# Optimization experiments

Measured on AMD Instinct MI355X. Metric: run time of the kernel, lower is better.

Reference implementation:

```python
import jax, jax.numpy as jnp
import numpy as np

B, S, D, T = 64, 128, 512, 64  # batch, encoder len, dim_model, longest_coor

def setup_inputs() -> dict:
    key = jax.random.key(0)
    ks = jax.random.split(key, 10)
    def rn(k, shape, s=0.02):
        return jax.random.normal(k, shape, dtype=jnp.float32) * s
    return dict(
        e_all=jax.random.normal(ks[0], (B, S, D), dtype=jnp.float32),
        e_last=jax.random.normal(ks[1], (1, B, D), dtype=jnp.float32),
        Wa_w=rn(ks[2], (D, D)), Wa_b=jnp.zeros((D,), jnp.float32),
        Ua_w=rn(ks[3], (D, D)), Ua_b=jnp.zeros((D,), jnp.float32),
        Va_w=rn(ks[4], (D, 1)), Va_b=jnp.zeros((1,), jnp.float32),
        W_ih=rn(ks[5], (3 * D, D + 3)),  # GRU input weights, input = cat(attn[D], coord[3])
        W_hh=rn(ks[6], (3 * D, D)),
        b_ih=jnp.zeros((3 * D,), jnp.float32),
        b_hh=jnp.zeros((3 * D,), jnp.float32),
        Wo_w=rn(ks[7], (D, 3)), Wo_b=jnp.zeros((3,), jnp.float32),
    )

def reference(e_all, e_last, Wa_w, Wa_b, Ua_w, Ua_b, Va_w, Va_b,
              W_ih, W_hh, b_ih, b_hh, Wo_w, Wo_b):
    # Ua(keys) is step-invariant: hoist out of the decode loop (same math).
    Uk = e_all @ Ua_w + Ua_b                      # [B,S,D]
    h0 = e_last[0]                                # [B,D]
    x0 = jnp.zeros((e_all.shape[0], 3), e_all.dtype)

    def step(carry, _):
        h, x = carry
        # Bahdanau attention: query = current hidden state
        q = h @ Wa_w + Wa_b                       # [B,D]
        scores = jnp.squeeze(jnp.tanh(q[:, None, :] + Uk) @ Va_w, -1) + Va_b  # [B,S]
        w = jax.nn.softmax(scores, axis=-1)       # [B,S]
        ctx = jnp.einsum('bs,bsd->bd', w, e_all)  # [B,D]
        # single-step GRU, input = cat(context, prev coord)
        gin = jnp.concatenate([ctx, x], axis=-1)  # [B,D+3]
        gi = gin @ W_ih.T + b_ih                  # [B,3D]
        gh = h @ W_hh.T + b_hh                    # [B,3D]
        gir, giz, gin_n = jnp.split(gi, 3, axis=-1)
        ghr, ghz, ghn = jnp.split(gh, 3, axis=-1)
        r = jax.nn.sigmoid(gir + ghr)
        z = jax.nn.sigmoid(giz + ghz)
        n = jnp.tanh(gin_n + r * ghn)
        h_new = (1.0 - z) * n + z * h             # [B,D]
        out = h_new @ Wo_w + Wo_b                 # [B,3]
        return (h_new, out), (out, w)

    (hT, _), (outs, attns) = jax.lax.scan(step, (h0, x0), None, length=T)
    d_outputs = jnp.transpose(outs, (1, 0, 2))    # [B,T,3]
    cross_attn = jnp.transpose(attns, (1, 0, 2))  # [B,T,S]
    return d_outputs, hT[None], cross_attn
```

## Files before the change

kernel.cpp:

```cpp
#include <hip/hip_runtime.h>

typedef unsigned int u32;
typedef unsigned long long u64;
typedef float f32x4 __attribute__((ext_vector_type(4)));
typedef short short8 __attribute__((ext_vector_type(8)));

#define OFF_UKB 0u
#define OFF_QX  16777216u
#define OFF_EX  17563648u
#define G_BYTES 102400u

#define OFF_OUT_HT  12288u
#define OFF_OUT_ATT 45056u

#define NBLK 192
#define NTHR 512
#define DYN_LDS 145408
#define PREP_LDS 36864

__device__ __forceinline__ float fast_rcp(float x) { return __builtin_amdgcn_rcpf(x); }
__device__ __forceinline__ float tanh5(float x) {
    float e = __expf(2.f * x);
    return 1.f - 2.f * fast_rcp(e + 1.f);
}
__device__ __forceinline__ float sigm_f(float x) { return fast_rcp(1.f + __expf(-x)); }

__device__ __forceinline__ u32 packbf2(float a, float b) {
    u32 ua = __float_as_uint(a); ua += 0x7FFFu + ((ua >> 16) & 1u);
    u32 ub = __float_as_uint(b); ub += 0x7FFFu + ((ub >> 16) & 1u);
    return (ua >> 16) | (ub & 0xFFFF0000u);
}
__device__ __forceinline__ float2 unpackbf2(u32 u) {
    return make_float2(__uint_as_float(u << 16), __uint_as_float(u & 0xFFFF0000u));
}
__device__ __forceinline__ float bf16hi(float x, float& lo) {
    u32 u = __float_as_uint(x); u += 0x7FFFu + ((u >> 16) & 1u); u &= 0xFFFF0000u;
    const float h = __uint_as_float(u); lo = x - h; return h;
}

__device__ __forceinline__ u64 cload64(const u64* p) {
    return __hip_atomic_load(p, __ATOMIC_RELAXED, __HIP_MEMORY_SCOPE_AGENT);
}
__device__ __forceinline__ void cstore64(u64* p, u64 v) {
    __hip_atomic_store(p, v, __ATOMIC_RELAXED, __HIP_MEMORY_SCOPE_AGENT);
}
__device__ __forceinline__ u32 cload32(const u32* p) {
    return __hip_atomic_load(p, __ATOMIC_RELAXED, __HIP_MEMORY_SCOPE_AGENT);
}
__device__ __forceinline__ void cstore32(u32* p, u32 v) {
    __hip_atomic_store(p, v, __ATOMIC_RELAXED, __HIP_MEMORY_SCOPE_AGENT);
}

union U8 { u32 u[4]; uint4 q; short8 s; };

__global__ __launch_bounds__(256) void prep_kernel(
    const float* __restrict__ e_all, const float* __restrict__ e_last,
    const float* __restrict__ Ua_w,  const float* __restrict__ Ua_b,
    float* __restrict__ ws)
{
    extern __shared__ char pls[];
    u32* Ahi = (u32*)pls;
    u32* Alo = Ahi + 64 * 36;
    u32* Bhi = Alo + 64 * 36;
    u32* Blo = Bhi + 64 * 36;

    u32* UKB = (u32*)((char*)ws + OFF_UKB);

    const int blk = blockIdx.x, tid = threadIdx.x;
    const int gtid = blk * 256 + tid, gstride = 1024 * 256;

    for (int i = gtid; i < 2048; i += gstride) {
        const int g = i >> 9, j = i & 511;
        ((u32*)((char*)ws + OFF_EX + (size_t)g * G_BYTES + 98304))[j] = 0u;
    }
    for (int i = gtid; i < 32768; i += gstride) {
        const int g = i >> 13, j = i & 8191;
        ((u64*)((char*)ws + OFF_EX + (size_t)g * G_BYTES + 32768))[j] = 0ull;
    }
    for (int i = gtid; i < 65536; i += gstride)
        ((u64*)((char*)ws + OFF_QX))[i] = 0ull;
    for (int i = gtid; i < 8192; i += gstride) {
        const int g = i >> 11, i2 = i & 2047;
        const float* ep = e_last + ((size_t)(g * 16 + (i2 >> 7)) * 512) + 4 * (i2 & 127);
        u64* HX = (u64*)((char*)ws + OFF_EX + (size_t)g * G_BYTES);
        HX[i2] = (u64)packbf2(ep[0], ep[1]) | ((u64)packbf2(ep[2], ep[3]) << 32);
    }

    const int r0 = (blk >> 3) * 64, c0 = (blk & 7) * 64;
    const int lane = tid & 63, wv = tid >> 6;
    const int mn = lane & 15, quad = lane >> 4;

    f32x4 acc[4];
    #pragma unroll
    for (int rg = 0; rg < 4; ++rg) acc[rg] = (f32x4){0.f, 0.f, 0.f, 0.f};

    for (int ks = 0; ks < 8; ++ks) {
        if (ks) __syncthreads();
        for (int i = tid; i < 1024; i += 256) {
            const int row = i >> 4, q4i = i & 15;
            const float4 e = *(const float4*)(e_all + (size_t)(r0 + row) * 512 + ks * 64 + 4 * q4i);
            float l0, l1, l2, l3;
            const float h0 = bf16hi(e.x, l0), h1 = bf16hi(e.y, l1);
            const float h2 = bf16hi(e.z, l2), h3 = bf16hi(e.w, l3);
            Ahi[row * 36 + 2 * q4i]     = packbf2(h0, h1);
            Ahi[row * 36 + 2 * q4i + 1] = packbf2(h2, h3);
            Alo[row * 36 + 2 * q4i]     = packbf2(l0, l1);
            Alo[row * 36 + 2 * q4i + 1] = packbf2(l2, l3);
        }
        for (int i = tid; i < 2048; i += 256) {
            const int col = i & 63, kp = i >> 6;
            const float b0 = Ua_w[(size_t)(ks * 64 + 2 * kp) * 512 + c0 + col];
            const float b1 = Ua_w[(size_t)(ks * 64 + 2 * kp + 1) * 512 + c0 + col];
            float l0, l1;
            const float h0 = bf16hi(b0, l0), h1 = bf16hi(b1, l1);
            Bhi[col * 36 + kp] = packbf2(h0, h1);
            Blo[col * 36 + kp] = packbf2(l0, l1);
        }
        __syncthreads();
        #pragma unroll
        for (int kb = 0; kb < 2; ++kb) {
            const int fo = kb * 16 + quad * 4;
            U8 bh, bl;
            bh.q = *(const uint4*)(Bhi + (wv * 16 + mn) * 36 + fo);
            bl.q = *(const uint4*)(Blo + (wv * 16 + mn) * 36 + fo);
            #pragma unroll
            for (int rg = 0; rg < 4; ++rg) {
                U8 ah, al;
                ah.q = *(const uint4*)(Ahi + (rg * 16 + mn) * 36 + fo);
                al.q = *(const uint4*)(Alo + (rg * 16 + mn) * 36 + fo);
                acc[rg] = __builtin_amdgcn_mfma_f32_16x16x32_bf16(al.s, bh.s, acc[rg], 0, 0, 0);
                acc[rg] = __builtin_amdgcn_mfma_f32_16x16x32_bf16(ah.s, bl.s, acc[rg], 0, 0, 0);
                acc[rg] = __builtin_amdgcn_mfma_f32_16x16x32_bf16(ah.s, bh.s, acc[rg], 0, 0, 0);
            }
        }
    }
    const int col = c0 + wv * 16 + mn;
    const float bias = Ua_b[col];
    #pragma unroll
    for (int rg = 0; rg < 4; ++rg) {
        #pragma unroll
        for (int reg = 0; reg < 4; ++reg) {
            const float v = acc[rg][reg] + bias;
            const float v1 = __shfl_down(v, 1);
            if (!(mn & 1))
                UKB[(size_t)(r0 + rg * 16 + quad * 4 + reg) * 256 + (col >> 1)] = packbf2(v, v1);
        }
    }
}

__global__ __launch_bounds__(512, 1) void decode_kernel(
    const float* __restrict__ e_all,
    const float* __restrict__ e_last,
    const float* __restrict__ Wa_w,  const float* __restrict__ Wa_b,
    const float* __restrict__ Va_w,
    const float* __restrict__ W_ih,  const float* __restrict__ W_hh,
    const float* __restrict__ b_ih,  const float* __restrict__ b_hh,
    const float* __restrict__ Wo_w,  const float* __restrict__ Wo_b,
    float* __restrict__ out, float* __restrict__ ws)
{
    extern __shared__ char smraw[];

    const u32* UKB = (const u32*)((char*)ws + OFF_UKB);

    const int tid = threadIdx.x;
    const int bi  = blockIdx.x;
    const int g   = bi / 48, r = bi % 48;
    const int lane = tid & 63, wv = tid >> 6;

    char* gbase = (char*)ws + OFF_EX + (size_t)g * G_BYTES;
    u64* HX = (u64*)gbase;
    u64* CX = (u64*)(gbase + 32768);
    u32* FH = (u32*)(gbase + 98304);

    if (r < 16) {
        const int bl = r, b = g * 16 + bl;
        u32*   EuL  = (u32*)smraw;
        float* eq_s = (float*)(smraw + 131072);
        float* w_s  = (float*)(smraw + 133120);
        float* red  = (float*)(smraw + 133632);
        float* psq  = (float*)(smraw + 133696);

        const u64* QXR = (const u64*)((char*)ws + OFF_QX + (size_t)g * 131072u);

        {
            const uint4* src = (const uint4*)(UKB + (size_t)b * 32768);
            uint4* dst = (uint4*)EuL;
            #pragma unroll
            for (int i = 0; i < 16; ++i) {
                uint4 u = src[tid + 512 * i];
                float2 p;
                p = unpackbf2(u.x); u.x = packbf2(__expf(2.f * p.x), __expf(2.f * p.y));
                p = unpackbf2(u.y); u.y = packbf2(__expf(2.f * p.x), __expf(2.f * p.y));
                p = unpackbf2(u.z); u.z = packbf2(__expf(2.f * p.x), __expf(2.f * p.y));
                p = unpackbf2(u.w); u.w = packbf2(__expf(2.f * p.x), __expf(2.f * p.y));
                dst[tid + 512 * i] = u;
            }
        }
        uint2 ereg[32];
        {
            const int dq = tid & 127, sg = tid >> 7;
            const float* ep = e_all + (size_t)b * 65536;
            #pragma unroll
            for (int si = 0; si < 32; ++si) {
                const float4 e = *(const float4*)(ep + (size_t)(sg * 32 + si) * 512 + 4 * dq);
                ereg[si] = make_uint2(packbf2(e.x, e.y), packbf2(e.z, e.w));
            }
        }
        const int kl = lane & 15;
        float4 va2a[4], va2b[4];
        float vaSum = 0.f;
        #pragma unroll
        for (int it = 0; it < 4; ++it) {
            const float4 a  = *(const float4*)(Va_w + (it * 16 + kl) * 8);
            const float4 b2 = *(const float4*)(Va_w + (it * 16 + kl) * 8 + 4);
            vaSum += a.x + a.y + a.z + a.w + b2.x + b2.y + b2.z + b2.w;
            va2a[it] = make_float4(-2.f * a.x,  -2.f * a.y,  -2.f * a.z,  -2.f * a.w);
            va2b[it] = make_float4(-2.f * b2.x, -2.f * b2.y, -2.f * b2.z, -2.f * b2.w);
        }
        __syncthreads();

        for (int t = 0; t < 64; ++t) {
            const int slot = t & 1;
            const u32 tg = (u32)(t + 1);
            u64* CxS = CX + slot * 4096;
            const u64* QxS = QXR + slot * 8192 + (size_t)bl * 512;

            if (tid < 256) {
                u64 v0 = cload64(QxS + 2 * tid), v1 = cload64(QxS + 2 * tid + 1);
                while ((u32)(v0 >> 32) != tg) v0 = cload64(QxS + 2 * tid);
                while ((u32)(v1 >> 32) != tg) v1 = cload64(QxS + 2 * tid + 1);
                ((float2*)eq_s)[tid] = make_float2(__uint_as_float((u32)v0),
                                                   __uint_as_float((u32)v1));
            }
            __syncthreads();

            {
                float4 eqa[4], eqb[4];
                const float4* q4 = (const float4*)eq_s;
                #pragma unroll
                for (int it = 0; it < 4; ++it) {
                    eqa[it] = q4[(it * 16 + kl) * 2];  eqb[it] = q4[(it * 16 + kl) * 2 + 1];
                }
                const int sbase = wv * 16 + (lane >> 4);
                #pragma unroll
                for (int sg = 0; sg < 4; ++sg) {
                    const int s = sbase + sg * 4;
                    const uint4* uk4 = (const uint4*)EuL + (size_t)s * 64;
                    float acc = vaSum;
                    #pragma unroll
                    for (int it = 0; it < 4; ++it) {
                        const uint4 u = uk4[it * 16 + kl];
                        const float2 u0 = unpackbf2(u.x), u1 = unpackbf2(u.y);
                        const float2 u2 = unpackbf2(u.z), u3 = unpackbf2(u.w);
                        acc = fmaf(va2a[it].x, fast_rcp(fmaf(eqa[it].x, u0.x, 1.f)), acc);
                        acc = fmaf(va2a[it].y, fast_rcp(fmaf(eqa[it].y, u0.y, 1.f)), acc);
                        acc = fmaf(va2a[it].z, fast_rcp(fmaf(eqa[it].z, u1.x, 1.f)), acc);
                        acc = fmaf(va2a[it].w, fast_rcp(fmaf(eqa[it].w, u1.y, 1.f)), acc);
                        acc = fmaf(va2b[it].x, fast_rcp(fmaf(eqb[it].x, u2.x, 1.f)), acc);
                        acc = fmaf(va2b[it].y, fast_rcp(fmaf(eqb[it].y, u2.y, 1.f)), acc);
                        acc = fmaf(va2b[it].z, fast_rcp(fmaf(eqb[it].z, u3.x, 1.f)), acc);
                        acc = fmaf(va2b[it].w, fast_rcp(fmaf(eqb[it].w, u3.y, 1.f)), acc);
                    }
                    acc += __shfl_xor(acc, 1); acc += __shfl_xor(acc, 2);
                    acc += __shfl_xor(acc, 4); acc += __shfl_xor(acc, 8);
                    if (kl == 0) w_s[s] = __expf(acc);
                }
            }
            __syncthreads();

            if (tid < 64) {
                float sm = w_s[tid] + w_s[tid + 64];
                #pragma unroll
                for (int off = 32; off > 0; off >>= 1) sm += __shfl_down(sm, off);
                if (tid == 0) red[1] = fast_rcp(sm);
            }
            {
                const int dq = tid & 127, sg = tid >> 7;
                float4 a = {0.f, 0.f, 0.f, 0.f};
                #pragma unroll
                for (int si = 0; si < 32; ++si) {
                    const float wgt = w_s[sg * 32 + si];
                    const float2 e0 = unpackbf2(ereg[si].x), e1 = unpackbf2(ereg[si].y);
                    a.x = fmaf(wgt, e0.x, a.x);
                    a.y = fmaf(wgt, e0.y, a.y);
                    a.z = fmaf(wgt, e1.x, a.z);
                    a.w = fmaf(wgt, e1.y, a.w);
                }
                ((float4*)psq)[sg * 128 + dq] = a;
            }
            __syncthreads();
            if (tid < 128) {
                const float rn = red[1];
                const float4* p4 = (const float4*)psq;
                float4 a = p4[tid], b2 = p4[128 + tid], c2 = p4[256 + tid], d2 = p4[384 + tid];
                const float rx = (a.x + b2.x + c2.x + d2.x) * rn;
                const float ry = (a.y + b2.y + c2.y + d2.y) * rn;
                const float rz = (a.z + b2.z + c2.z + d2.z) * rn;
                const float rw = (a.w + b2.w + c2.w + d2.w) * rn;
                const u64 tg64 = (u64)tg << 32;
                cstore64(CxS + (size_t)bl * 256 + 2 * tid,     tg64 | (u64)packbf2(rx, ry));
                cstore64(CxS + (size_t)bl * 256 + 2 * tid + 1, tg64 | (u64)packbf2(rz, rw));
            } else if (tid < 256) {
                out[OFF_OUT_ATT + ((size_t)b * 64 + t) * 128 + (tid - 128)] = w_s[tid - 128] * red[1];
            }
        }
    } else {
        const int idx = r - 16, d0 = idx * 16;
        u32*   hbu  = (u32*)smraw;
        u32*   cbu  = (u32*)(smraw + 16640);
        float* gh_s = (float*)(smraw + 33280);
        float* gi_s = (float*)(smraw + 36352);
        float* x_s  = (float*)(smraw + 39424);
        float* wx_s = (float*)(smraw + 39616);
        float* wo_s = (float*)(smraw + 40192);

        u64* QXW = (u64*)((char*)ws + OFF_QX + (size_t)g * 131072u);

        const int mn = lane & 15, quad = lane >> 4;

        short8 bfrag[16];
        float qbias = 0.f;
        if (wv < 3) {
            const float* wrow = W_hh + (size_t)(wv * 512 + d0 + mn) * 512;
            #pragma unroll
            for (int kb = 0; kb < 16; ++kb) {
                const int k0 = kb * 32 + quad * 8;
                U8 tpk;
                #pragma unroll
                for (int c = 0; c < 4; ++c)
                    tpk.u[c] = packbf2(wrow[k0 + 2 * c], wrow[k0 + 2 * c + 1]);
                bfrag[kb] = tpk.s;
            }
        } else if (wv < 6) {
            const float* wrow = W_ih + (size_t)((wv - 3) * 512 + d0 + mn) * 515;
            #pragma unroll
            for (int kb = 0; kb < 16; ++kb) {
                const int k0 = kb * 32 + quad * 8;
                U8 tpk;
                #pragma unroll
                for (int c = 0; c < 4; ++c)
                    tpk.u[c] = packbf2(wrow[k0 + 2 * c], wrow[k0 + 2 * c + 1]);
                bfrag[kb] = tpk.s;
            }
        } else if (wv == 6) {
            #pragma unroll
            for (int kb = 0; kb < 16; ++kb) {
                const int k0 = kb * 32 + quad * 8;
                U8 tpk;
                #pragma unroll
                for (int c = 0; c < 4; ++c)
                    tpk.u[c] = packbf2(Wa_w[(size_t)(k0 + 2 * c) * 512 + d0 + mn],
                                       Wa_w[(size_t)(k0 + 2 * c + 1) * 512 + d0 + mn]);
                bfrag[kb] = tpk.s;
            }
            qbias = Wa_b[d0 + mn];
        }
        if (tid < 144) {
            const int dd = tid / 9, rem = tid - dd * 9, g3 = rem / 3, c = rem - g3 * 3;
            wx_s[tid] = W_ih[(size_t)(g3 * 512 + d0 + dd) * 515 + 512 + c];
        }
        for (int i = tid; i < 1536; i += 512) wo_s[i] = Wo_w[i];
        if (tid < 3) wo_s[1536 + tid] = Wo_b[tid];

        const int gb = tid >> 4, gd = tid & 15;
        float hold = 0.f, bih[3], bhh[3];
        if (tid < 256) {
            hold = e_last[(size_t)(g * 16 + gb) * 512 + d0 + gd];
            #pragma unroll
            for (int g3 = 0; g3 < 3; ++g3) {
                bih[g3] = b_ih[g3 * 512 + d0 + gd];
                bhh[g3] = b_hh[g3 * 512 + d0 + gd];
            }
        }

        for (int t = 0; t < 64; ++t) {
            const int slot = t & 1;
            const u32 tg = (u32)(t + 1);
            const u64* HxS = HX + slot * 2048;
            const u64* CxS = CX + slot * 4096;
            u64* HxW = HX + ((t + 1) & 1) * 2048;

            if (lane < 16) {
                const u32* f = FH + ((wv & 1) * 16 + lane) * 16;
                while (cload32(f) < (u32)t) {}
            }
            #pragma unroll
            for (int u = 0; u < 4; ++u) {
                const int i = tid + 512 * u;
                const u64 v = cload64(HxS + i);
                *(u64*)(hbu + (i >> 7) * 260 + (i & 127) * 2) = v;
            }
            __syncthreads();

            if (wv < 3) {
                f32x4 c = {0.f, 0.f, 0.f, 0.f};
                #pragma unroll
                for (int kb = 0; kb < 16; ++kb) {
                    U8 a; a.q = *(const uint4*)(hbu + mn * 260 + kb * 16 + quad * 4);
                    c = __builtin_amdgcn_mfma_f32_16x16x32_bf16(a.s, bfrag[kb], c, 0, 0, 0);
                }
                #pragma unroll
                for (int reg = 0; reg < 4; ++reg)
                    gh_s[((quad * 4 + reg) * 16 + mn) * 3 + wv] = c[reg];
            } else if (wv == 7) {
                const int tt = tid - 448, cb = tt >> 2, kl = tt & 3;
                if (t > 0) {
                    float a0 = 0.f, a1 = 0.f, a2 = 0.f;
                    #pragma unroll 4
                    for (int c = 0; c < 64; ++c) {
                        const int p = kl * 64 + c;
                        const float2 hv = unpackbf2(hbu[cb * 260 + p]);
                        const float* w0 = wo_s + 2 * p * 3;
                        a0 = fmaf(hv.x, w0[0], fmaf(hv.y, w0[3], a0));
                        a1 = fmaf(hv.x, w0[1], fmaf(hv.y, w0[4], a1));
                        a2 = fmaf(hv.x, w0[2], fmaf(hv.y, w0[5], a2));
                    }
                    a0 += __shfl_xor(a0, 1); a1 += __shfl_xor(a1, 1); a2 += __shfl_xor(a2, 1);
                    a0 += __shfl_xor(a0, 2); a1 += __shfl_xor(a1, 2); a2 += __shfl_xor(a2, 2);
                    if (kl == 0) {
                        x_s[cb * 3 + 0] = a0 + wo_s[1536];
                        x_s[cb * 3 + 1] = a1 + wo_s[1537];
                        x_s[cb * 3 + 2] = a2 + wo_s[1538];
                    }
                } else if (tt < 48) x_s[tt] = 0.f;
            } else {
                if (wv == 6) {
                    f32x4 c = {0.f, 0.f, 0.f, 0.f};
                    #pragma unroll
                    for (int kb = 0; kb < 16; ++kb) {
                        U8 a; a.q = *(const uint4*)(hbu + mn * 260 + kb * 16 + quad * 4);
                        c = __builtin_amdgcn_mfma_f32_16x16x32_bf16(a.s, bfrag[kb], c, 0, 0, 0);
                    }
                    u64* QxW = QXW + slot * 8192;
                    const u64 tg64 = (u64)tg << 32;
                    #pragma unroll
                    for (int reg = 0; reg < 4; ++reg) {
                        const float q0 = c[reg] + qbias;
                        const float e  = __expf(2.f * q0);
                        cstore64(QxW + (size_t)(quad * 4 + reg) * 512 + d0 + mn,
                                 tg64 | (u64)__float_as_uint(e));
                    }
                }
                const int thr = (wv - 3) * 64 + lane;
                u64 cc[16];
                u32 pend = 0xFFFFu;
                #pragma unroll
                for (int k = 0; k < 16; ++k) cc[k] = cload64(CxS + thr + 256 * k);
                #pragma unroll
                for (int k = 0; k < 16; ++k)
                    if ((u32)(cc[k] >> 32) == tg) { cbu[k * 260 + thr] = (u32)cc[k]; pend &= ~(1u << k); }
                while (pend) {
                    #pragma unroll
                    for (int k = 0; k < 16; ++k)
                        if (pend & (1u << k)) cc[k] = cload64(CxS + thr + 256 * k);
                    #pragma unroll
                    for (int k = 0; k < 16; ++k)
                        if ((pend & (1u << k)) && (u32)(cc[k] >> 32) == tg) {
                            cbu[k * 260 + thr] = (u32)cc[k]; pend &= ~(1u << k);
                        }
                }
            }
            __syncthreads();

            if (wv >= 3 && wv < 6) {
                f32x4 c = {0.f, 0.f, 0.f, 0.f};
                #pragma unroll
                for (int kb = 0; kb < 16; ++kb) {
                    U8 a; a.q = *(const uint4*)(cbu + mn * 260 + kb * 16 + quad * 4);
                    c = __builtin_amdgcn_mfma_f32_16x16x32_bf16(a.s, bfrag[kb], c, 0, 0, 0);
                }
                #pragma unroll
                for (int reg = 0; reg < 4; ++reg)
                    gi_s[((quad * 4 + reg) * 16 + mn) * 3 + (wv - 3)] = c[reg];
            } else if (idx == 0 && t > 0 && tid < 48) {
                out[((size_t)(g * 16 + tid / 3) * 64 + (t - 1)) * 3 + tid % 3] = x_s[tid];
            }
            __syncthreads();

            if (tid < 256) {
                const int ob = (gb * 16 + gd) * 3;
                const float x0 = x_s[gb * 3 + 0], x1 = x_s[gb * 3 + 1], x2 = x_s[gb * 3 + 2];
                const float giR = gi_s[ob + 0] + bih[0]
                                + x0 * wx_s[gd * 9 + 0] + x1 * wx_s[gd * 9 + 1] + x2 * wx_s[gd * 9 + 2];
                const float giZ = gi_s[ob + 1] + bih[1]
                                + x0 * wx_s[gd * 9 + 3] + x1 * wx_s[gd * 9 + 4] + x2 * wx_s[gd * 9 + 5];
                const float giN = gi_s[ob + 2] + bih[2]
                                + x0 * wx_s[gd * 9 + 6] + x1 * wx_s[gd * 9 + 7] + x2 * wx_s[gd * 9 + 8];
                const float ghR = gh_s[ob + 0] + bhh[0];
                const float ghZ = gh_s[ob + 1] + bhh[1];
                const float ghN = gh_s[ob + 2] + bhh[2];
                const float rg = sigm_f(giR + ghR);
                const float zg = sigm_f(giZ + ghZ);
                const float ng = tanh5(giN + rg * ghN);
                const float hnew = (1.f - zg) * ng + zg * hold;
                hold = hnew;
                const float s1 = __shfl_down(hnew, 1);
                const float s2 = __shfl_down(hnew, 2);
                const float s3 = __shfl_down(hnew, 3);
                if ((gd & 3) == 0)
                    cstore64(HxW + gb * 128 + ((d0 + gd) >> 2),
                             (u64)packbf2(hnew, s1) | ((u64)packbf2(s2, s3) << 32));
                if (t == 63)
                    out[OFF_OUT_HT + (size_t)(g * 16 + gb) * 512 + d0 + gd] = hnew;
            }
            __syncthreads();
            if (tid == 0) cstore32(FH + idx * 16, (u32)(t + 1));
        }

        if (tid < 32) { const u32* f = FH + tid * 16; while (cload32(f) < 64u) {} }
        __syncthreads();
        #pragma unroll
        for (int u = 0; u < 4; ++u) {
            const int i = tid + 512 * u;
            const u64 v = cload64(HX + i);
            *(u64*)(hbu + (i >> 7) * 260 + (i & 127) * 2) = v;
        }
        __syncthreads();
        if (wv >= 6) {
            const int tt = tid - 384, cb = tt >> 3, kl = tt & 7;
            float a0 = 0.f, a1 = 0.f, a2 = 0.f;
            #pragma unroll 4
            for (int c = 0; c < 32; ++c) {
                const int p = kl * 32 + c;
                const float2 hv = unpackbf2(hbu[cb * 260 + p]);
                const float* w0 = wo_s + 2 * p * 3;
                a0 = fmaf(hv.x, w0[0], fmaf(hv.y, w0[3], a0));
                a1 = fmaf(hv.x, w0[1], fmaf(hv.y, w0[4], a1));
                a2 = fmaf(hv.x, w0[2], fmaf(hv.y, w0[5], a2));
            }
            a0 += __shfl_xor(a0, 1); a1 += __shfl_xor(a1, 1); a2 += __shfl_xor(a2, 1);
            a0 += __shfl_xor(a0, 2); a1 += __shfl_xor(a1, 2); a2 += __shfl_xor(a2, 2);
            a0 += __shfl_xor(a0, 4); a1 += __shfl_xor(a1, 4); a2 += __shfl_xor(a2, 4);
            if (kl == 0) {
                x_s[cb * 3 + 0] = a0 + wo_s[1536];
                x_s[cb * 3 + 1] = a1 + wo_s[1537];
                x_s[cb * 3 + 2] = a2 + wo_s[1538];
            }
        }
        __syncthreads();
        if (idx == 0 && tid < 48)
            out[((size_t)(g * 16 + tid / 3) * 64 + 63) * 3 + tid % 3] = x_s[tid];
    }
}

extern "C" void kernel_launch(void* const* d_in, const int* in_sizes, int n_in,
                              void* d_out, int out_size, void* d_ws, size_t ws_size,
                              hipStream_t stream) {
    const float* e_all  = (const float*)d_in[0];
    const float* e_last = (const float*)d_in[1];
    const float* Wa_w   = (const float*)d_in[2];
    const float* Wa_b   = (const float*)d_in[3];
    const float* Ua_w   = (const float*)d_in[4];
    const float* Ua_b   = (const float*)d_in[5];
    const float* Va_w   = (const float*)d_in[6];
    const float* W_ih   = (const float*)d_in[8];
    const float* W_hh   = (const float*)d_in[9];
    const float* b_ih   = (const float*)d_in[10];
    const float* b_hh   = (const float*)d_in[11];
    const float* Wo_w   = (const float*)d_in[12];
    const float* Wo_b   = (const float*)d_in[13];
    float* outp = (float*)d_out;
    float* ws   = (float*)d_ws;

    hipFuncSetAttribute((const void*)prep_kernel,
                        hipFuncAttributeMaxDynamicSharedMemorySize, PREP_LDS);
    hipFuncSetAttribute((const void*)decode_kernel,
                        hipFuncAttributeMaxDynamicSharedMemorySize, DYN_LDS);

    hipLaunchKernelGGL(prep_kernel, dim3(1024), dim3(256), PREP_LDS, stream,
                       e_all, e_last, Ua_w, Ua_b, ws);

    void* args[] = { (void*)&e_all, (void*)&e_last, (void*)&Wa_w, (void*)&Wa_b,
                     (void*)&Va_w,
                     (void*)&W_ih, (void*)&W_hh, (void*)&b_ih, (void*)&b_hh,
                     (void*)&Wo_w, (void*)&Wo_b, (void*)&outp, (void*)&ws };
    hipError_t err = hipLaunchCooperativeKernel((void*)decode_kernel, dim3(NBLK), dim3(NTHR),
                                                args, DYN_LDS, stream);
    if (err != hipSuccess) {
        hipLaunchKernelGGL(decode_kernel, dim3(NBLK), dim3(NTHR), DYN_LDS, stream,
                           e_all, e_last, Wa_w, Wa_b, Va_w,
                           W_ih, W_hh, b_ih, b_hh, Wo_w, Wo_b, outp, ws);
    }
}
```

Measured before the change: 839.1 us.

## Replace per-block flag barriers with step-tagged hidden-state words

The hidden-state exchange between GRU blocks now embeds the step number in the upper 32 bits of each 64-bit word, with the packed bf16 pair in the lower half. Readers spin on the individual words until the tag matches, instead of waiting on per-block completion flags. This removes the trailing __syncthreads and flag store per step, and the flag polling before reading. In exchange the exchange buffer doubles, each thread issues twice as many 64-bit loads, and polling may spin per element.

```diff
diff --git a/kernel.cpp b/kernel.cpp
--- a/kernel.cpp
+++ b/kernel.cpp
@@ -8,7 +8,7 @@
 #define OFF_UKB 0u
 #define OFF_QX  16777216u
 #define OFF_EX  17563648u
-#define G_BYTES 102400u
+#define G_BYTES 131072u
 
 #define OFF_OUT_HT  12288u
 #define OFF_OUT_ATT 45056u
@@ -42,12 +42,6 @@
     return __hip_atomic_load(p, __ATOMIC_RELAXED, __HIP_MEMORY_SCOPE_AGENT);
 }
 __device__ __forceinline__ void cstore64(u64* p, u64 v) {
-    __hip_atomic_store(p, v, __ATOMIC_RELAXED, __HIP_MEMORY_SCOPE_AGENT);
-}
-__device__ __forceinline__ u32 cload32(const u32* p) {
-    return __hip_atomic_load(p, __ATOMIC_RELAXED, __HIP_MEMORY_SCOPE_AGENT);
-}
-__device__ __forceinline__ void cstore32(u32* p, u32 v) {
     __hip_atomic_store(p, v, __ATOMIC_RELAXED, __HIP_MEMORY_SCOPE_AGENT);
 }
 
@@ -69,21 +63,22 @@
     const int blk = blockIdx.x, tid = threadIdx.x;
     const int gtid = blk * 256 + tid, gstride = 1024 * 256;
 
-    for (int i = gtid; i < 2048; i += gstride) {
-        const int g = i >> 9, j = i & 511;
-        ((u32*)((char*)ws + OFF_EX + (size_t)g * G_BYTES + 98304))[j] = 0u;
+    for (int i = gtid; i < 16384; i += gstride) {
+        const int g = i >> 12, j = i & 4095;
+        ((u64*)((char*)ws + OFF_EX + (size_t)g * G_BYTES))[4096 + j] = 0ull;
     }
     for (int i = gtid; i < 32768; i += gstride) {
         const int g = i >> 13, j = i & 8191;
-        ((u64*)((char*)ws + OFF_EX + (size_t)g * G_BYTES + 32768))[j] = 0ull;
+        ((u64*)((char*)ws + OFF_EX + (size_t)g * G_BYTES + 65536))[j] = 0ull;
     }
     for (int i = gtid; i < 65536; i += gstride)
         ((u64*)((char*)ws + OFF_QX))[i] = 0ull;
-    for (int i = gtid; i < 8192; i += gstride) {
-        const int g = i >> 11, i2 = i & 2047;
-        const float* ep = e_last + ((size_t)(g * 16 + (i2 >> 7)) * 512) + 4 * (i2 & 127);
-        u64* HX = (u64*)((char*)ws + OFF_EX + (size_t)g * G_BYTES);
-        HX[i2] = (u64)packbf2(ep[0], ep[1]) | ((u64)packbf2(ep[2], ep[3]) << 32);
+    for (int i = gtid; i < 16384; i += gstride) {
+        const int g = i >> 12, i2 = i & 4095;
+        const int b = i2 >> 8, pr = i2 & 255;
+        const float* ep = e_last + ((size_t)(g * 16 + b) * 512) + 2 * pr;
+        u64* HXg = (u64*)((char*)ws + OFF_EX + (size_t)g * G_BYTES);
+        HXg[i2] = (u64)packbf2(ep[0], ep[1]);
     }
 
     const int r0 = (blk >> 3) * 64, c0 = (blk & 7) * 64;
@@ -169,8 +164,7 @@
 
     char* gbase = (char*)ws + OFF_EX + (size_t)g * G_BYTES;
     u64* HX = (u64*)gbase;
-    u64* CX = (u64*)(gbase + 32768);
-    u32* FH = (u32*)(gbase + 98304);
+    u64* CX = (u64*)(gbase + 65536);
 
     if (r < 16) {
         const int bl = r, b = g * 16 + bl;
@@ -376,19 +370,35 @@
         for (int t = 0; t < 64; ++t) {
             const int slot = t & 1;
             const u32 tg = (u32)(t + 1);
-            const u64* HxS = HX + slot * 2048;
+            const u64* HxS = HX + slot * 4096;
             const u64* CxS = CX + slot * 4096;
-            u64* HxW = HX + ((t + 1) & 1) * 2048;
-
-            if (lane < 16) {
-                const u32* f = FH + ((wv & 1) * 16 + lane) * 16;
-                while (cload32(f) < (u32)t) {}
-            }
-            #pragma unroll
-            for (int u = 0; u < 4; ++u) {
-                const int i = tid + 512 * u;
-                const u64 v = cload64(HxS + i);
-                *(u64*)(hbu + (i >> 7) * 260 + (i & 127) * 2) = v;
+            u64* HxW = HX + ((t + 1) & 1) * 4096;
+
+            {
+                const u32 htag = (u32)t;
+                u64 hh[8];
+                u32 pend = 0xFFu;
+                #pragma unroll
+                for (int k = 0; k < 8; ++k) hh[k] = cload64(HxS + tid + 512 * k);
+                #pragma unroll
+                for (int k = 0; k < 8; ++k)
+                    if ((u32)(hh[k] >> 32) == htag) {
+                        const int i = tid + 512 * k;
+                        hbu[(i >> 8) * 260 + (i & 255)] = (u32)hh[k];
+                        pend &= ~(1u << k);
+                    }
+                while (pend) {
+                    #pragma unroll
+                    for (int k = 0; k < 8; ++k)
+                        if (pend & (1u << k)) hh[k] = cload64(HxS + tid + 512 * k);
+                    #pragma unroll
+                    for (int k = 0; k < 8; ++k)
+                        if ((pend & (1u << k)) && (u32)(hh[k] >> 32) == htag) {
+                            const int i = tid + 512 * k;
+                            hbu[(i >> 8) * 260 + (i & 255)] = (u32)hh[k];
+                            pend &= ~(1u << k);
+                        }
+                }
             }
             __syncthreads();
 
@@ -495,25 +505,38 @@
                 const float hnew = (1.f - zg) * ng + zg * hold;
                 hold = hnew;
                 const float s1 = __shfl_down(hnew, 1);
-                const float s2 = __shfl_down(hnew, 2);
-                const float s3 = __shfl_down(hnew, 3);
-                if ((gd & 3) == 0)
-                    cstore64(HxW + gb * 128 + ((d0 + gd) >> 2),
-                             (u64)packbf2(hnew, s1) | ((u64)packbf2(s2, s3) << 32));
+                if ((gd & 1) == 0)
+                    cstore64(HxW + (size_t)gb * 256 + ((d0 + gd) >> 1),
+                             ((u64)tg << 32) | (u64)packbf2(hnew, s1));
                 if (t == 63)
                     out[OFF_OUT_HT + (size_t)(g * 16 + gb) * 512 + d0 + gd] = hnew;
             }
-            __syncthreads();
-            if (tid == 0) cstore32(FH + idx * 16, (u32)(t + 1));
-        }
-
-        if (tid < 32) { const u32* f = FH + tid * 16; while (cload32(f) < 64u) {} }
-        __syncthreads();
-        #pragma unroll
-        for (int u = 0; u < 4; ++u) {
-            const int i = tid + 512 * u;
-            const u64 v = cload64(HX + i);
-            *(u64*)(hbu + (i >> 7) * 260 + (i & 127) * 2) = v;
+        }
+
+        {
+            u64 hh[8];
+            u32 pend = 0xFFu;
+            #pragma unroll
+            for (int k = 0; k < 8; ++k) hh[k] = cload64(HX + tid + 512 * k);
+            #pragma unroll
+            for (int k = 0; k < 8; ++k)
+                if ((u32)(hh[k] >> 32) == 64u) {
+                    const int i = tid + 512 * k;
+                    hbu[(i >> 8) * 260 + (i & 255)] = (u32)hh[k];
+                    pend &= ~(1u << k);
+                }
+            while (pend) {
+                #pragma unroll
+                for (int k = 0; k < 8; ++k)
+                    if (pend & (1u << k)) hh[k] = cload64(HX + tid + 512 * k);
+                #pragma unroll
+                for (int k = 0; k < 8; ++k)
+                    if ((pend & (1u << k)) && (u32)(hh[k] >> 32) == 64u) {
+                        const int i = tid + 512 * k;
+                        hbu[(i >> 8) * 260 + (i & 255)] = (u32)hh[k];
+                        pend &= ~(1u << k);
+                    }
+            }
         }
         __syncthreads();
         if (wv >= 6) {
```

After: 832.4 us. No clear change (-0.8%).
